# Optimization experiments

Measured on AMD Instinct MI355X. Metric: run time of the kernel, lower is better.

The kernel has to match this reference:

```python
import jax, jax.numpy as jnp
import numpy as np

N = 100000          # nodes
E = 1600000         # edges (avg degree 16)
C = 40              # classes
NUM_CORRECT = 10
ALPHA_CORRECT = 0.9
NUM_SMOOTH = 10
ALPHA_SMOOTH = 0.8


def setup_inputs() -> dict:
    key = jax.random.key(0)
    k1, k2, k3, k4, k5 = jax.random.split(key, 5)
    y_true = jax.random.randint(k1, (N,), 0, C, dtype=jnp.int32)
    y_soft = jax.nn.softmax(jax.random.normal(k2, (N, C), dtype=jnp.float32), axis=-1)
    spread_mask = jax.random.bernoulli(k3, 0.5, (N,))
    edge_index = jax.random.randint(k4, (2, E), 0, N, dtype=jnp.int32)
    edge_weight = jax.random.uniform(k5, (E,), dtype=jnp.float32)
    return {"y_true": y_true, "y_soft": y_soft, "spread_mask": spread_mask,
            "edge_index": edge_index, "edge_weight": edge_weight}


def _gcn_norm(edge_index, edge_weight):
    # symmetric normalization D^-1/2 A D^-1/2 (no self loops, as in PyG LabelPropagation)
    row, col = edge_index[0], edge_index[1]
    deg = jax.ops.segment_sum(edge_weight, row, num_segments=N)
    dis = jnp.where(deg > 0, jax.lax.rsqrt(deg), 0.0)  # deg^-0.5 with inf -> 0
    norm = dis[row] * edge_weight * dis[col]
    return row, col, norm


def _propagate(x0, row, col, norm, alpha, num_layers, post_step):
    def step(x, _):
        agg = jax.ops.segment_sum(norm[:, None] * x[col], row, num_segments=N)
        x = alpha * agg + (1.0 - alpha) * x
        return post_step(x), None
    x, _ = jax.lax.scan(step, x0, None, length=num_layers)
    return x


def reference(y_true, y_soft, spread_mask, edge_index, edge_weight):
    row, col, norm = _gcn_norm(edge_index, edge_weight)
    y_oh = jax.nn.one_hot(y_true, C, dtype=y_soft.dtype)
    mask = spread_mask[:, None]

    # ---- correct ----
    error = jnp.where(mask, y_oh - y_soft, 0.0)  # zeros off-mask, like scatter
    smoothed = _propagate(error, row, col, norm, ALPHA_CORRECT, NUM_CORRECT,
                          lambda x: jnp.clip(x, -1.0, 1.0))
    numel = spread_mask.sum().astype(y_soft.dtype)
    sigma = jnp.abs(error).sum() / numel  # error is zero outside mask
    denom = jnp.abs(smoothed).sum(axis=1, keepdims=True)
    raw = sigma / jnp.where(denom > 0, denom, 1.0)
    scale = jnp.where((denom <= 0) | (raw > 1000.0), 1.0, raw)
    y_corr = y_soft + scale * smoothed

    # ---- smooth ----
    y_s = jnp.where(mask, y_oh, y_corr)  # inject true labels at spread nodes
    out = _propagate(y_s, row, col, norm, ALPHA_SMOOTH, NUM_SMOOTH,
                     lambda y: jax.nn.softmax(y, axis=-1))
    return out
```

## Files before the change

### kernel.cpp

```cpp
#include <hip/hip_runtime.h>
#include <hip/hip_fp16.h>
#include <math.h>

#define C_CLS 40
#define RPB 6

struct __align__(8) H4 { __half2 a; __half2 b; };

static __device__ __forceinline__ float h15f(unsigned b) {
  union { unsigned short s; __half h; } u;
  u.s = (unsigned short)b;
  return __half2float(u.h);
}
static __device__ __forceinline__ unsigned f2h15(float w) {
  union { __half h; unsigned short s; } u;
  u.h = __float2half_rn(w);
  return (unsigned)u.s;
}

static __device__ __forceinline__ bool load_mask(const void* p, int esz, int i) {
  if (esz == 1) return ((const unsigned char*)p)[i] != 0;
  return ((const unsigned int*)p)[i] != 0u;
}

__global__ void detect_kernel(const unsigned int* m, int* flag) {
  __shared__ int bad;
  if (threadIdx.x == 0) bad = 0;
  __syncthreads();
  unsigned int v = m[threadIdx.x];
  if (!(v == 0u || v == 1u || v == 0x3F800000u)) bad = 1;
  __syncthreads();
  if (threadIdx.x == 0) flag[0] = bad ? 1 : 4;
}

__global__ void hist_kernel(const int* __restrict__ row, int* __restrict__ cnt, int E) {
  int e = blockIdx.x * blockDim.x + threadIdx.x;
  if (e < E) atomicAdd(&cnt[row[e]], 1);
}

__global__ void scan1_kernel(const int* __restrict__ cnt, int* __restrict__ rp,
                             int* __restrict__ part, int n) {
  __shared__ int sh[256];
  int gid = blockIdx.x * 256 + threadIdx.x;
  int v = (gid < n) ? cnt[gid] : 0;
  sh[threadIdx.x] = v;
  __syncthreads();
  for (int o = 1; o < 256; o <<= 1) {
    int t = (threadIdx.x >= o) ? sh[threadIdx.x - o] : 0;
    __syncthreads();
    sh[threadIdx.x] += t;
    __syncthreads();
  }
  if (gid < n) rp[gid] = sh[threadIdx.x] - v;
  if (threadIdx.x == 255) part[blockIdx.x] = sh[255];
}

__global__ void scan2_kernel(int* part, int B) {
  __shared__ int sh[1024];
  int t = threadIdx.x;
  int v = (t < B) ? part[t] : 0;
  sh[t] = v;
  __syncthreads();
  for (int o = 1; o < 1024; o <<= 1) {
    int u = (t >= o) ? sh[t - o] : 0;
    __syncthreads();
    sh[t] += u;
    __syncthreads();
  }
  if (t < B) part[t] = sh[t] - v;
}

__global__ void scan3_kernel(int* __restrict__ rp, int* __restrict__ cur,
                             const int* __restrict__ part, int n, int E) {
  int gid = blockIdx.x * 256 + threadIdx.x;
  if (gid < n) {
    int v = rp[gid] + part[blockIdx.x];
    rp[gid] = v;
    cur[gid] = v;
  }
  if (gid == 0) rp[n] = E;
}

__global__ void scatter_kernel(const int* __restrict__ row, const int* __restrict__ col,
                               const float* __restrict__ w,
                               int* __restrict__ cursor, unsigned* __restrict__ eg, int E) {
  int e = blockIdx.x * blockDim.x + threadIdx.x;
  if (e < E) {
    int r = row[e];
    int pos = atomicAdd(&cursor[r], 1);
    eg[pos] = (unsigned)col[e] | (f2h15(w[e]) << 17);
  }
}

__global__ void deg_rsqrt_kernel(const unsigned* __restrict__ eg, const int* __restrict__ rp,
                                 float* __restrict__ dis, int n) {
  int i = blockIdx.x * blockDim.x + threadIdx.x;
  if (i < n) {
    float s = 0.f;
    int e1 = rp[i + 1];
    for (int e = rp[i]; e < e1; ++e) s += h15f(eg[e] >> 17);
    dis[i] = (s > 0.f) ? rsqrtf(s) : 0.f;
  }
}

__global__ void norm_kernel(unsigned* __restrict__ eg, const int* __restrict__ rp,
                            const float* __restrict__ dis, int n) {
  int i = blockIdx.x * blockDim.x + threadIdx.x;
  if (i < n) {
    float dr = dis[i];
    int e1 = rp[i + 1];
    for (int e = rp[i]; e < e1; ++e) {
      unsigned u = eg[e];
      unsigned c = u & 0x1FFFFu;
      float w = dr * h15f(u >> 17) * dis[c];
      eg[e] = c | (f2h15(w) << 17);
    }
  }
}

__global__ void __launch_bounds__(256) init_error_kernel(
    H4* __restrict__ x16, const float4* __restrict__ ysoft4,
    const int* __restrict__ ytrue, const void* maskp,
    const int* __restrict__ flag, float* __restrict__ sig,
    int* __restrict__ numel, int n) {
  const int esz = flag[0];
  const int total = n * 10;
  float asum = 0.f;
  int cnt = 0;
  for (int q = blockIdx.x * blockDim.x + threadIdx.x; q < total;
       q += gridDim.x * blockDim.x) {
    int i = q / 10;
    int c4 = q - i * 10;
    float4 e = make_float4(0.f, 0.f, 0.f, 0.f);
    if (load_mask(maskp, esz, i)) {
      float4 p = ysoft4[q];
      int t = ytrue[i];
      int cb = c4 * 4;
      e.x = ((t == cb) ? 1.f : 0.f) - p.x;
      e.y = ((t == cb + 1) ? 1.f : 0.f) - p.y;
      e.z = ((t == cb + 2) ? 1.f : 0.f) - p.z;
      e.w = ((t == cb + 3) ? 1.f : 0.f) - p.w;
      if (c4 == 0) cnt++;
    }
    H4 h;
    h.a = __floats2half2_rn(e.x, e.y);
    h.b = __floats2half2_rn(e.z, e.w);
    x16[i * 16 + c4] = h;
    asum += fabsf(e.x) + fabsf(e.y) + fabsf(e.z) + fabsf(e.w);
  }
  for (int o = 32; o > 0; o >>= 1) {
    asum += __shfl_down(asum, o);
    cnt += __shfl_down(cnt, o);
  }
  __shared__ float swf[4];
  __shared__ int swi[4];
  int lane = threadIdx.x & 63, wv = threadIdx.x >> 6;
  if (lane == 0) { swf[wv] = asum; swi[wv] = cnt; }
  __syncthreads();
  if (threadIdx.x == 0) {
    atomicAdd(sig, swf[0] + swf[1] + swf[2] + swf[3]);
    atomicAdd(numel, swi[0] + swi[1] + swi[2] + swi[3]);
  }
}

__global__ void __launch_bounds__(320) prop_h_clip(const H4* __restrict__ xin,
                                                   H4* __restrict__ xout,
                                                   const int* __restrict__ rp,
                                                   const unsigned* __restrict__ eg,
                                                   float alpha, int n) {
  const int t = threadIdx.x;
  const int lr = t / 10;
  const int c4 = t - lr * 10;
  const int i = blockIdx.x * 32 + lr;
  if (i >= n) return;
  int e0 = rp[i], e1 = rp[i + 1];
  H4 hs = xin[i * 16 + c4];
  float2 s0 = __half22float2(hs.a), s1 = __half22float2(hs.b);
  float4 acc = make_float4(0.f, 0.f, 0.f, 0.f);
  int e = e0;
  for (; e + 3 < e1; e += 4) {
    unsigned u0 = eg[e], u1 = eg[e + 1], u2 = eg[e + 2], u3 = eg[e + 3];
    H4 h0 = xin[(u0 & 0x1FFFFu) * 16 + c4];
    H4 h1 = xin[(u1 & 0x1FFFFu) * 16 + c4];
    H4 h2 = xin[(u2 & 0x1FFFFu) * 16 + c4];
    H4 h3 = xin[(u3 & 0x1FFFFu) * 16 + c4];
    float w0 = h15f(u0 >> 17), w1 = h15f(u1 >> 17),
          w2 = h15f(u2 >> 17), w3 = h15f(u3 >> 17);
    float2 a0 = __half22float2(h0.a), b0 = __half22float2(h0.b);
    float2 a1 = __half22float2(h1.a), b1 = __half22float2(h1.b);
    float2 a2 = __half22float2(h2.a), b2 = __half22float2(h2.b);
    float2 a3 = __half22float2(h3.a), b3 = __half22float2(h3.b);
    acc.x = fmaf(w0, a0.x, acc.x); acc.y = fmaf(w0, a0.y, acc.y);
    acc.z = fmaf(w0, b0.x, acc.z); acc.w = fmaf(w0, b0.y, acc.w);
    acc.x = fmaf(w1, a1.x, acc.x); acc.y = fmaf(w1, a1.y, acc.y);
    acc.z = fmaf(w1, b1.x, acc.z); acc.w = fmaf(w1, b1.y, acc.w);
    acc.x = fmaf(w2, a2.x, acc.x); acc.y = fmaf(w2, a2.y, acc.y);
    acc.z = fmaf(w2, b2.x, acc.z); acc.w = fmaf(w2, b2.y, acc.w);
    acc.x = fmaf(w3, a3.x, acc.x); acc.y = fmaf(w3, a3.y, acc.y);
    acc.z = fmaf(w3, b3.x, acc.z); acc.w = fmaf(w3, b3.y, acc.w);
  }
  for (; e < e1; ++e) {
    unsigned u = eg[e];
    H4 h = xin[(u & 0x1FFFFu) * 16 + c4];
    float w = h15f(u >> 17);
    float2 a = __half22float2(h.a), b = __half22float2(h.b);
    acc.x = fmaf(w, a.x, acc.x); acc.y = fmaf(w, a.y, acc.y);
    acc.z = fmaf(w, b.x, acc.z); acc.w = fmaf(w, b.y, acc.w);
  }
  float beta = 1.f - alpha;
  float vx = fminf(1.f, fmaxf(-1.f, alpha * acc.x + beta * s0.x));
  float vy = fminf(1.f, fmaxf(-1.f, alpha * acc.y + beta * s0.y));
  float vz = fminf(1.f, fmaxf(-1.f, alpha * acc.z + beta * s1.x));
  float vw = fminf(1.f, fmaxf(-1.f, alpha * acc.w + beta * s1.y));
  H4 o;
  o.a = __floats2half2_rn(vx, vy);
  o.b = __floats2half2_rn(vz, vw);
  xout[i * 16 + c4] = o;
}

template <int OUT16>
__global__ void __launch_bounds__(320) prop_h_soft(const H4* __restrict__ xin,
                                                   void* __restrict__ xout,
                                                   const int* __restrict__ rp,
                                                   const unsigned* __restrict__ eg,
                                                   float alpha, int n) {
  const int t = threadIdx.x;
  const int lr = t / 10;
  const int c4 = t - lr * 10;
  const int i = blockIdx.x * 32 + lr;
  const bool active = (i < n);
  float4 v = make_float4(0.f, 0.f, 0.f, 0.f);
  if (active) {
    int e0 = rp[i], e1 = rp[i + 1];
    H4 hs = xin[i * 16 + c4];
    float2 s0 = __half22float2(hs.a), s1 = __half22float2(hs.b);
    float4 acc = make_float4(0.f, 0.f, 0.f, 0.f);
    int e = e0;
    for (; e + 3 < e1; e += 4) {
      unsigned u0 = eg[e], u1 = eg[e + 1], u2 = eg[e + 2], u3 = eg[e + 3];
      H4 h0 = xin[(u0 & 0x1FFFFu) * 16 + c4];
      H4 h1 = xin[(u1 & 0x1FFFFu) * 16 + c4];
      H4 h2 = xin[(u2 & 0x1FFFFu) * 16 + c4];
      H4 h3 = xin[(u3 & 0x1FFFFu) * 16 + c4];
      float w0 = h15f(u0 >> 17), w1 = h15f(u1 >> 17),
            w2 = h15f(u2 >> 17), w3 = h15f(u3 >> 17);
      float2 a0 = __half22float2(h0.a), b0 = __half22float2(h0.b);
      float2 a1 = __half22float2(h1.a), b1 = __half22float2(h1.b);
      float2 a2 = __half22float2(h2.a), b2 = __half22float2(h2.b);
      float2 a3 = __half22float2(h3.a), b3 = __half22float2(h3.b);
      acc.x = fmaf(w0, a0.x, acc.x); acc.y = fmaf(w0, a0.y, acc.y);
      acc.z = fmaf(w0, b0.x, acc.z); acc.w = fmaf(w0, b0.y, acc.w);
      acc.x = fmaf(w1, a1.x, acc.x); acc.y = fmaf(w1, a1.y, acc.y);
      acc.z = fmaf(w1, b1.x, acc.z); acc.w = fmaf(w1, b1.y, acc.w);
      acc.x = fmaf(w2, a2.x, acc.x); acc.y = fmaf(w2, a2.y, acc.y);
      acc.z = fmaf(w2, b2.x, acc.z); acc.w = fmaf(w2, b2.y, acc.w);
      acc.x = fmaf(w3, a3.x, acc.x); acc.y = fmaf(w3, a3.y, acc.y);
      acc.z = fmaf(w3, b3.x, acc.z); acc.w = fmaf(w3, b3.y, acc.w);
    }
    for (; e < e1; ++e) {
      unsigned u = eg[e];
      H4 h = xin[(u & 0x1FFFFu) * 16 + c4];
      float w = h15f(u >> 17);
      float2 a = __half22float2(h.a), b = __half22float2(h.b);
      acc.x = fmaf(w, a.x, acc.x); acc.y = fmaf(w, a.y, acc.y);
      acc.z = fmaf(w, b.x, acc.z); acc.w = fmaf(w, b.y, acc.w);
    }
    float beta = 1.f - alpha;
    v.x = alpha * acc.x + beta * s0.x;
    v.y = alpha * acc.y + beta * s0.y;
    v.z = alpha * acc.z + beta * s1.x;
    v.w = alpha * acc.w + beta * s1.y;
  }
  __shared__ float sh[32][10];
  __shared__ float shr[32];
  float lmax = fmaxf(fmaxf(v.x, v.y), fmaxf(v.z, v.w));
  if (active) sh[lr][c4] = lmax;
  __syncthreads();
  if (active && c4 == 0) {
    float m = sh[lr][0];
#pragma unroll
    for (int k = 1; k < 10; ++k) m = fmaxf(m, sh[lr][k]);
    shr[lr] = m;
  }
  __syncthreads();
  float m = active ? shr[lr] : 0.f;
  float ex = __expf(v.x - m), ey = __expf(v.y - m),
        ez = __expf(v.z - m), ew = __expf(v.w - m);
  if (active) sh[lr][c4] = ex + ey + ez + ew;
  __syncthreads();
  if (active && c4 == 0) {
    float s = sh[lr][0];
#pragma unroll
    for (int k = 1; k < 10; ++k) s += sh[lr][k];
    shr[lr] = s;
  }
  __syncthreads();
  if (active) {
    float inv = 1.f / shr[lr];
    if (OUT16) {
      H4 o;
      o.a = __floats2half2_rn(ex * inv, ey * inv);
      o.b = __floats2half2_rn(ez * inv, ew * inv);
      ((H4*)xout)[i * 16 + c4] = o;
    } else {
      ((float4*)xout)[i * 10 + c4] =
          make_float4(ex * inv, ey * inv, ez * inv, ew * inv);
    }
  }
}

__global__ void __launch_bounds__(256) scale_kernel(const __half* __restrict__ smh,
                                                    __half* __restrict__ outh,
                                                    const float* __restrict__ ysoft,
                                                    const int* __restrict__ ytrue,
                                                    const void* maskp,
                                                    const int* __restrict__ flag,
                                                    const float* __restrict__ sig,
                                                    const int* __restrict__ numel, int n) {
  int t = threadIdx.x;
  int lr = t / C_CLS, c = t - lr * C_CLS;
  int i = blockIdx.x * RPB + lr;
  bool active = (lr < RPB) && (i < n);
  __shared__ float sh[RPB][C_CLS];
  __shared__ float shd[RPB];
  float v = 0.f;
  if (active) {
    v = __half2float(smh[i * 64 + c]);
    sh[lr][c] = fabsf(v);
  }
  __syncthreads();
  if (active && c == 0) {
    float d = 0.f;
#pragma unroll
    for (int k = 0; k < C_CLS; ++k) d += sh[lr][k];
    shd[lr] = d;
  }
  __syncthreads();
  if (active) {
    float denom = shd[lr];
    float sigma = sig[0] / (float)numel[0];
    float raw = sigma / ((denom > 0.f) ? denom : 1.f);
    float scale = (denom <= 0.f || raw > 1000.f) ? 1.f : raw;
    float yc = ysoft[i * C_CLS + c] + scale * v;
    float oh = (ytrue[i] == c) ? 1.f : 0.f;
    float ys = load_mask(maskp, flag[0], i) ? oh : yc;
    outh[i * 64 + c] = __float2half_rn(ys);
  }
}

extern "C" void kernel_launch(void* const* d_in, const int* in_sizes, int n_in,
                              void* d_out, int out_size, void* d_ws, size_t ws_size,
                              hipStream_t stream) {
  const int* y_true = (const int*)d_in[0];
  const float* y_soft = (const float*)d_in[1];
  const void* maskp = d_in[2];
  const int* ei = (const int*)d_in[3];
  const float* ew = (const float*)d_in[4];
  const int n = in_sizes[0];
  const int E = in_sizes[4];
  const int* row = ei;
  const int* col = ei + E;

  char* ws = (char*)d_ws;
  size_t o = 0;
  auto alloc = [&](size_t bytes) -> void* {
    void* p = ws + o;
    o += (bytes + 255) & ~(size_t)255;
    return p;
  };
  H4* xA16 = (H4*)alloc((size_t)n * 128);
  unsigned* eg = (unsigned*)alloc((size_t)E * 4);
  float* dis = (float*)alloc((size_t)n * 4);
  int* cnt = (int*)alloc((size_t)n * 4);
  float* sig = (float*)alloc(4);
  int* numel = (int*)alloc(4);
  int* flag = (int*)alloc(4);
  int* rp = (int*)alloc((size_t)(n + 1) * 4);
  int* cur = (int*)alloc((size_t)n * 4);
  int* part = (int*)alloc(4096);
  H4* out16 = (H4*)d_out;

  hipMemsetAsync(cnt, 0, (size_t)n * 4, stream);
  hipMemsetAsync(sig, 0, 4, stream);
  hipMemsetAsync(numel, 0, 4, stream);

  const int be = (E + 255) / 256;
  const int bn = (n + 255) / 256;
  const int bp = (n + 31) / 32;
  const int bsc = (n + RPB - 1) / RPB;

  detect_kernel<<<1, 256, 0, stream>>>((const unsigned int*)maskp, flag);
  hist_kernel<<<be, 256, 0, stream>>>(row, cnt, E);
  scan1_kernel<<<bn, 256, 0, stream>>>(cnt, rp, part, n);
  scan2_kernel<<<1, 1024, 0, stream>>>(part, bn);
  scan3_kernel<<<bn, 256, 0, stream>>>(rp, cur, part, n, E);
  scatter_kernel<<<be, 256, 0, stream>>>(row, col, ew, cur, eg, E);
  deg_rsqrt_kernel<<<bn, 256, 0, stream>>>(eg, rp, dis, n);
  norm_kernel<<<bn, 256, 0, stream>>>(eg, rp, dis, n);
  init_error_kernel<<<512, 256, 0, stream>>>(xA16, (const float4*)y_soft,
                                             y_true, maskp, flag, sig, numel, n);

  H4* ha = xA16;
  H4* hb = out16;
  for (int k = 0; k < 10; ++k) {
    prop_h_clip<<<bp, 320, 0, stream>>>(ha, hb, rp, eg, 0.9f, n);
    H4* t = ha; ha = hb; hb = t;
  }
  scale_kernel<<<bsc, 256, 0, stream>>>((const __half*)ha, (__half*)d_out, y_soft,
                                        y_true, maskp, flag, sig, numel, n);

  ha = out16;
  hb = xA16;
  for (int k = 0; k < 9; ++k) {
    prop_h_soft<1><<<bp, 320, 0, stream>>>(ha, (void*)hb, rp, eg, 0.8f, n);
    H4* t = ha; ha = hb; hb = t;
  }
  prop_h_soft<0><<<bp, 320, 0, stream>>>(ha, d_out, rp, eg, 0.8f, n);
}
```

Measured before the change: 998.8 us.

## Split each propagation step into two column-half gather passes for cache locality

Each row's CSR edges are partitioned by whether the source column is in the lower or upper half of the node range, so every propagation step becomes two passes. The first gathers from the lower half into an fp16 temporary and the second gathers from the upper half and applies the update. This shrinks the gather working set per pass so it fits better in L2/MALL. In exchange it doubles the kernel launches, adds a temporary write and read, adds an extra fp16 rounding of the partial sums, and makes the CSR build scan twice as many segments.

```diff
diff --git a/kernel.cpp b/kernel.cpp
--- a/kernel.cpp
+++ b/kernel.cpp
@@ -33,16 +33,17 @@
   if (threadIdx.x == 0) flag[0] = bad ? 1 : 4;
 }
 
-__global__ void hist_kernel(const int* __restrict__ row, int* __restrict__ cnt, int E) {
+__global__ void hist_kernel(const int* __restrict__ row, const int* __restrict__ col,
+                            int* __restrict__ cnt2, int E, int half) {
   int e = blockIdx.x * blockDim.x + threadIdx.x;
-  if (e < E) atomicAdd(&cnt[row[e]], 1);
+  if (e < E) atomicAdd(&cnt2[(row[e] << 1) | (col[e] >= half ? 1 : 0)], 1);
 }
 
 __global__ void scan1_kernel(const int* __restrict__ cnt, int* __restrict__ rp,
-                             int* __restrict__ part, int n) {
+                             int* __restrict__ part, int n2) {
   __shared__ int sh[256];
   int gid = blockIdx.x * 256 + threadIdx.x;
-  int v = (gid < n) ? cnt[gid] : 0;
+  int v = (gid < n2) ? cnt[gid] : 0;
   sh[threadIdx.x] = v;
   __syncthreads();
   for (int o = 1; o < 256; o <<= 1) {
@@ -51,7 +52,7 @@
     sh[threadIdx.x] += t;
     __syncthreads();
   }
-  if (gid < n) rp[gid] = sh[threadIdx.x] - v;
+  if (gid < n2) rp[gid] = sh[threadIdx.x] - v;
   if (threadIdx.x == 255) part[blockIdx.x] = sh[255];
 }
 
@@ -71,45 +72,45 @@
 }
 
 __global__ void scan3_kernel(int* __restrict__ rp, int* __restrict__ cur,
-                             const int* __restrict__ part, int n, int E) {
+                             const int* __restrict__ part, int n2, int E) {
   int gid = blockIdx.x * 256 + threadIdx.x;
-  if (gid < n) {
+  if (gid < n2) {
     int v = rp[gid] + part[blockIdx.x];
     rp[gid] = v;
     cur[gid] = v;
   }
-  if (gid == 0) rp[n] = E;
+  if (gid == 0) rp[n2] = E;
 }
 
 __global__ void scatter_kernel(const int* __restrict__ row, const int* __restrict__ col,
-                               const float* __restrict__ w,
-                               int* __restrict__ cursor, unsigned* __restrict__ eg, int E) {
+                               const float* __restrict__ w, int* __restrict__ cursor,
+                               unsigned* __restrict__ eg, int E, int half) {
   int e = blockIdx.x * blockDim.x + threadIdx.x;
   if (e < E) {
-    int r = row[e];
-    int pos = atomicAdd(&cursor[r], 1);
-    eg[pos] = (unsigned)col[e] | (f2h15(w[e]) << 17);
-  }
-}
-
-__global__ void deg_rsqrt_kernel(const unsigned* __restrict__ eg, const int* __restrict__ rp,
+    int r = row[e], c = col[e];
+    int pos = atomicAdd(&cursor[(r << 1) | (c >= half ? 1 : 0)], 1);
+    eg[pos] = (unsigned)c | (f2h15(w[e]) << 17);
+  }
+}
+
+__global__ void deg_rsqrt_kernel(const unsigned* __restrict__ eg, const int* __restrict__ rp2,
                                  float* __restrict__ dis, int n) {
   int i = blockIdx.x * blockDim.x + threadIdx.x;
   if (i < n) {
     float s = 0.f;
-    int e1 = rp[i + 1];
-    for (int e = rp[i]; e < e1; ++e) s += h15f(eg[e] >> 17);
+    int e1 = rp2[2 * i + 2];
+    for (int e = rp2[2 * i]; e < e1; ++e) s += h15f(eg[e] >> 17);
     dis[i] = (s > 0.f) ? rsqrtf(s) : 0.f;
   }
 }
 
-__global__ void norm_kernel(unsigned* __restrict__ eg, const int* __restrict__ rp,
+__global__ void norm_kernel(unsigned* __restrict__ eg, const int* __restrict__ rp2,
                             const float* __restrict__ dis, int n) {
   int i = blockIdx.x * blockDim.x + threadIdx.x;
   if (i < n) {
     float dr = dis[i];
-    int e1 = rp[i + 1];
-    for (int e = rp[i]; e < e1; ++e) {
+    int e1 = rp2[2 * i + 2];
+    for (int e = rp2[2 * i]; e < e1; ++e) {
       unsigned u = eg[e];
       unsigned c = u & 0x1FFFFu;
       float w = dr * h15f(u >> 17) * dis[c];
@@ -163,20 +164,9 @@
   }
 }
 
-__global__ void __launch_bounds__(320) prop_h_clip(const H4* __restrict__ xin,
-                                                   H4* __restrict__ xout,
-                                                   const int* __restrict__ rp,
-                                                   const unsigned* __restrict__ eg,
-                                                   float alpha, int n) {
-  const int t = threadIdx.x;
-  const int lr = t / 10;
-  const int c4 = t - lr * 10;
-  const int i = blockIdx.x * 32 + lr;
-  if (i >= n) return;
-  int e0 = rp[i], e1 = rp[i + 1];
-  H4 hs = xin[i * 16 + c4];
-  float2 s0 = __half22float2(hs.a), s1 = __half22float2(hs.b);
-  float4 acc = make_float4(0.f, 0.f, 0.f, 0.f);
+static __device__ __forceinline__ void gather_acc(const H4* __restrict__ xin, int c4,
+                                                  const unsigned* __restrict__ eg,
+                                                  int e0, int e1, float4& acc) {
   int e = e0;
   for (; e + 3 < e1; e += 4) {
     unsigned u0 = eg[e], u1 = eg[e + 1], u2 = eg[e + 2], u3 = eg[e + 3];
@@ -207,23 +197,32 @@
     acc.x = fmaf(w, a.x, acc.x); acc.y = fmaf(w, a.y, acc.y);
     acc.z = fmaf(w, b.x, acc.z); acc.w = fmaf(w, b.y, acc.w);
   }
-  float beta = 1.f - alpha;
-  float vx = fminf(1.f, fmaxf(-1.f, alpha * acc.x + beta * s0.x));
-  float vy = fminf(1.f, fmaxf(-1.f, alpha * acc.y + beta * s0.y));
-  float vz = fminf(1.f, fmaxf(-1.f, alpha * acc.z + beta * s1.x));
-  float vw = fminf(1.f, fmaxf(-1.f, alpha * acc.w + beta * s1.y));
+}
+
+__global__ void __launch_bounds__(320) prop_pass0(const H4* __restrict__ xin,
+                                                  H4* __restrict__ tmp,
+                                                  const int* __restrict__ rp2,
+                                                  const unsigned* __restrict__ eg, int n) {
+  const int t = threadIdx.x;
+  const int lr = t / 10;
+  const int c4 = t - lr * 10;
+  const int i = blockIdx.x * 32 + lr;
+  if (i >= n) return;
+  float4 acc = make_float4(0.f, 0.f, 0.f, 0.f);
+  gather_acc(xin, c4, eg, rp2[2 * i], rp2[2 * i + 1], acc);
   H4 o;
-  o.a = __floats2half2_rn(vx, vy);
-  o.b = __floats2half2_rn(vz, vw);
-  xout[i * 16 + c4] = o;
-}
-
-template <int OUT16>
-__global__ void __launch_bounds__(320) prop_h_soft(const H4* __restrict__ xin,
-                                                   void* __restrict__ xout,
-                                                   const int* __restrict__ rp,
-                                                   const unsigned* __restrict__ eg,
-                                                   float alpha, int n) {
+  o.a = __floats2half2_rn(acc.x, acc.y);
+  o.b = __floats2half2_rn(acc.z, acc.w);
+  tmp[i * 10 + c4] = o;
+}
+
+template <int POST, int OUT16>
+__global__ void __launch_bounds__(320) prop_pass1(const H4* __restrict__ xin,
+                                                  void* __restrict__ xout,
+                                                  const H4* __restrict__ tmp,
+                                                  const int* __restrict__ rp2,
+                                                  const unsigned* __restrict__ eg,
+                                                  float alpha, int n) {
   const int t = threadIdx.x;
   const int lr = t / 10;
   const int c4 = t - lr * 10;
@@ -231,80 +230,63 @@
   const bool active = (i < n);
   float4 v = make_float4(0.f, 0.f, 0.f, 0.f);
   if (active) {
-    int e0 = rp[i], e1 = rp[i + 1];
+    H4 hp = tmp[i * 10 + c4];
+    float2 p0 = __half22float2(hp.a), p1 = __half22float2(hp.b);
+    float4 acc = make_float4(p0.x, p0.y, p1.x, p1.y);
+    gather_acc(xin, c4, eg, rp2[2 * i + 1], rp2[2 * i + 2], acc);
     H4 hs = xin[i * 16 + c4];
     float2 s0 = __half22float2(hs.a), s1 = __half22float2(hs.b);
-    float4 acc = make_float4(0.f, 0.f, 0.f, 0.f);
-    int e = e0;
-    for (; e + 3 < e1; e += 4) {
-      unsigned u0 = eg[e], u1 = eg[e + 1], u2 = eg[e + 2], u3 = eg[e + 3];
-      H4 h0 = xin[(u0 & 0x1FFFFu) * 16 + c4];
-      H4 h1 = xin[(u1 & 0x1FFFFu) * 16 + c4];
-      H4 h2 = xin[(u2 & 0x1FFFFu) * 16 + c4];
-      H4 h3 = xin[(u3 & 0x1FFFFu) * 16 + c4];
-      float w0 = h15f(u0 >> 17), w1 = h15f(u1 >> 17),
-            w2 = h15f(u2 >> 17), w3 = h15f(u3 >> 17);
-      float2 a0 = __half22float2(h0.a), b0 = __half22float2(h0.b);
-      float2 a1 = __half22float2(h1.a), b1 = __half22float2(h1.b);
-      float2 a2 = __half22float2(h2.a), b2 = __half22float2(h2.b);
-      float2 a3 = __half22float2(h3.a), b3 = __half22float2(h3.b);
-      acc.x = fmaf(w0, a0.x, acc.x); acc.y = fmaf(w0, a0.y, acc.y);
-      acc.z = fmaf(w0, b0.x, acc.z); acc.w = fmaf(w0, b0.y, acc.w);
-      acc.x = fmaf(w1, a1.x, acc.x); acc.y = fmaf(w1, a1.y, acc.y);
-      acc.z = fmaf(w1, b1.x, acc.z); acc.w = fmaf(w1, b1.y, acc.w);
-      acc.x = fmaf(w2, a2.x, acc.x); acc.y = fmaf(w2, a2.y, acc.y);
-      acc.z = fmaf(w2, b2.x, acc.z); acc.w = fmaf(w2, b2.y, acc.w);
-      acc.x = fmaf(w3, a3.x, acc.x); acc.y = fmaf(w3, a3.y, acc.y);
-      acc.z = fmaf(w3, b3.x, acc.z); acc.w = fmaf(w3, b3.y, acc.w);
-    }
-    for (; e < e1; ++e) {
-      unsigned u = eg[e];
-      H4 h = xin[(u & 0x1FFFFu) * 16 + c4];
-      float w = h15f(u >> 17);
-      float2 a = __half22float2(h.a), b = __half22float2(h.b);
-      acc.x = fmaf(w, a.x, acc.x); acc.y = fmaf(w, a.y, acc.y);
-      acc.z = fmaf(w, b.x, acc.z); acc.w = fmaf(w, b.y, acc.w);
-    }
     float beta = 1.f - alpha;
     v.x = alpha * acc.x + beta * s0.x;
     v.y = alpha * acc.y + beta * s0.y;
     v.z = alpha * acc.z + beta * s1.x;
     v.w = alpha * acc.w + beta * s1.y;
   }
-  __shared__ float sh[32][10];
-  __shared__ float shr[32];
-  float lmax = fmaxf(fmaxf(v.x, v.y), fmaxf(v.z, v.w));
-  if (active) sh[lr][c4] = lmax;
-  __syncthreads();
-  if (active && c4 == 0) {
-    float m = sh[lr][0];
+  if (POST == 0) {
+    if (active) {
+      H4 o;
+      o.a = __floats2half2_rn(fminf(1.f, fmaxf(-1.f, v.x)),
+                              fminf(1.f, fmaxf(-1.f, v.y)));
+      o.b = __floats2half2_rn(fminf(1.f, fmaxf(-1.f, v.z)),
+                              fminf(1.f, fmaxf(-1.f, v.w)));
+      ((H4*)xout)[i * 16 + c4] = o;
+    }
+  } else {
+    __shared__ float sh[32][10];
+    __shared__ float shr[32];
+    float lmax = fmaxf(fmaxf(v.x, v.y), fmaxf(v.z, v.w));
+    if (active) sh[lr][c4] = lmax;
+    __syncthreads();
+    if (active && c4 == 0) {
+      float m = sh[lr][0];
 #pragma unroll
-    for (int k = 1; k < 10; ++k) m = fmaxf(m, sh[lr][k]);
-    shr[lr] = m;
-  }
-  __syncthreads();
-  float m = active ? shr[lr] : 0.f;
-  float ex = __expf(v.x - m), ey = __expf(v.y - m),
-        ez = __expf(v.z - m), ew = __expf(v.w - m);
-  if (active) sh[lr][c4] = ex + ey + ez + ew;
-  __syncthreads();
-  if (active && c4 == 0) {
-    float s = sh[lr][0];
+      for (int k = 1; k < 10; ++k) m = fmaxf(m, sh[lr][k]);
+      shr[lr] = m;
+    }
+    __syncthreads();
+    float m = active ? shr[lr] : 0.f;
+    float ex = __expf(v.x - m), ey = __expf(v.y - m),
+          ez = __expf(v.z - m), ew = __expf(v.w - m);
+    if (active) sh[lr][c4] = ex + ey + ez + ew;
+    __syncthreads();
+    if (active && c4 == 0) {
+      float s = sh[lr][0];
 #pragma unroll
-    for (int k = 1; k < 10; ++k) s += sh[lr][k];
-    shr[lr] = s;
-  }
-  __syncthreads();
-  if (active) {
-    float inv = 1.f / shr[lr];
-    if (OUT16) {
-      H4 o;
-      o.a = __floats2half2_rn(ex * inv, ey * inv);
-      o.b = __floats2half2_rn(ez * inv, ew * inv);
-      ((H4*)xout)[i * 16 + c4] = o;
-    } else {
-      ((float4*)xout)[i * 10 + c4] =
-          make_float4(ex * inv, ey * inv, ez * inv, ew * inv);
+      for (int k = 1; k < 10; ++k) s += sh[lr][k];
+      shr[lr] = s;
+    }
+    __syncthreads();
+    if (active) {
+      float inv = 1.f / shr[lr];
+      if (OUT16) {
+        H4 o;
+        o.a = __floats2half2_rn(ex * inv, ey * inv);
+        o.b = __floats2half2_rn(ez * inv, ew * inv);
+        ((H4*)xout)[i * 16 + c4] = o;
+      } else {
+        ((float4*)xout)[i * 10 + c4] =
+            make_float4(ex * inv, ey * inv, ez * inv, ew * inv);
+      }
     }
   }
 }
@@ -360,6 +342,8 @@
   const int E = in_sizes[4];
   const int* row = ei;
   const int* col = ei + E;
+  const int half = n / 2;
+  const int n2 = 2 * n;
 
   char* ws = (char*)d_ws;
   size_t o = 0;
@@ -369,41 +353,44 @@
     return p;
   };
   H4* xA16 = (H4*)alloc((size_t)n * 128);
+  H4* tmp = (H4*)alloc((size_t)n * 80);
   unsigned* eg = (unsigned*)alloc((size_t)E * 4);
   float* dis = (float*)alloc((size_t)n * 4);
-  int* cnt = (int*)alloc((size_t)n * 4);
+  int* cnt2 = (int*)alloc((size_t)n2 * 4);
   float* sig = (float*)alloc(4);
   int* numel = (int*)alloc(4);
   int* flag = (int*)alloc(4);
-  int* rp = (int*)alloc((size_t)(n + 1) * 4);
-  int* cur = (int*)alloc((size_t)n * 4);
+  int* rp2 = (int*)alloc((size_t)(n2 + 1) * 4);
+  int* cur2 = (int*)alloc((size_t)n2 * 4);
   int* part = (int*)alloc(4096);
   H4* out16 = (H4*)d_out;
 
-  hipMemsetAsync(cnt, 0, (size_t)n * 4, stream);
+  hipMemsetAsync(cnt2, 0, (size_t)n2 * 4, stream);
   hipMemsetAsync(sig, 0, 4, stream);
   hipMemsetAsync(numel, 0, 4, stream);
 
   const int be = (E + 255) / 256;
   const int bn = (n + 255) / 256;
+  const int bn2 = (n2 + 255) / 256;
   const int bp = (n + 31) / 32;
   const int bsc = (n + RPB - 1) / RPB;
 
   detect_kernel<<<1, 256, 0, stream>>>((const unsigned int*)maskp, flag);
-  hist_kernel<<<be, 256, 0, stream>>>(row, cnt, E);
-  scan1_kernel<<<bn, 256, 0, stream>>>(cnt, rp, part, n);
-  scan2_kernel<<<1, 1024, 0, stream>>>(part, bn);
-  scan3_kernel<<<bn, 256, 0, stream>>>(rp, cur, part, n, E);
-  scatter_kernel<<<be, 256, 0, stream>>>(row, col, ew, cur, eg, E);
-  deg_rsqrt_kernel<<<bn, 256, 0, stream>>>(eg, rp, dis, n);
-  norm_kernel<<<bn, 256, 0, stream>>>(eg, rp, dis, n);
+  hist_kernel<<<be, 256, 0, stream>>>(row, col, cnt2, E, half);
+  scan1_kernel<<<bn2, 256, 0, stream>>>(cnt2, rp2, part, n2);
+  scan2_kernel<<<1, 1024, 0, stream>>>(part, bn2);
+  scan3_kernel<<<bn2, 256, 0, stream>>>(rp2, cur2, part, n2, E);
+  scatter_kernel<<<be, 256, 0, stream>>>(row, col, ew, cur2, eg, E, half);
+  deg_rsqrt_kernel<<<bn, 256, 0, stream>>>(eg, rp2, dis, n);
+  norm_kernel<<<bn, 256, 0, stream>>>(eg, rp2, dis, n);
   init_error_kernel<<<512, 256, 0, stream>>>(xA16, (const float4*)y_soft,
                                              y_true, maskp, flag, sig, numel, n);
 
   H4* ha = xA16;
   H4* hb = out16;
   for (int k = 0; k < 10; ++k) {
-    prop_h_clip<<<bp, 320, 0, stream>>>(ha, hb, rp, eg, 0.9f, n);
+    prop_pass0<<<bp, 320, 0, stream>>>(ha, tmp, rp2, eg, n);
+    prop_pass1<0, 1><<<bp, 320, 0, stream>>>(ha, (void*)hb, tmp, rp2, eg, 0.9f, n);
     H4* t = ha; ha = hb; hb = t;
   }
   scale_kernel<<<bsc, 256, 0, stream>>>((const __half*)ha, (__half*)d_out, y_soft,
@@ -412,8 +399,10 @@
   ha = out16;
   hb = xA16;
   for (int k = 0; k < 9; ++k) {
-    prop_h_soft<1><<<bp, 320, 0, stream>>>(ha, (void*)hb, rp, eg, 0.8f, n);
+    prop_pass0<<<bp, 320, 0, stream>>>(ha, tmp, rp2, eg, n);
+    prop_pass1<1, 1><<<bp, 320, 0, stream>>>(ha, (void*)hb, tmp, rp2, eg, 0.8f, n);
     H4* t = ha; ha = hb; hb = t;
   }
-  prop_h_soft<0><<<bp, 320, 0, stream>>>(ha, d_out, rp, eg, 0.8f, n);
-}
+  prop_pass0<<<bp, 320, 0, stream>>>(ha, tmp, rp2, eg, n);
+  prop_pass1<1, 0><<<bp, 320, 0, stream>>>(ha, d_out, tmp, rp2, eg, 0.8f, n);
+}
```

New measurement: 1.147 ms. 14.8% more time.
